# Performance work log

Measured on AMD Instinct MI355X. Metric: run time of the kernel, lower is better.

## Reference

```python
import jax, jax.numpy as jnp
import numpy as np

N_NODES = 50000


def gcn_conv(x, edge_index, W, b):
    """PyG GCNConv: add self-loops, symmetric deg^{-1/2} norm, W then aggregate."""
    n = x.shape[0]
    loops = jnp.arange(n, dtype=edge_index.dtype)
    src = jnp.concatenate([edge_index[0], loops])  # message sources
    dst = jnp.concatenate([edge_index[1], loops])  # aggregation targets
    h = x @ W  # [N, out_dim] -- transform before gather (PyG order)
    deg = jax.ops.segment_sum(jnp.ones_like(dst, dtype=h.dtype), dst, num_segments=n)
    dinv = jnp.where(deg > 0, jax.lax.rsqrt(jnp.maximum(deg, 1.0)), 0.0)
    norm = dinv[src] * dinv[dst]  # [E+N]
    msg = h[src] * norm[:, None]  # gather + normalize
    out = jax.ops.segment_sum(msg, dst, num_segments=n)  # scatter-add
    return out + b


def setup_inputs() -> dict:
    key = jax.random.key(0)
    k1, k2, k3, k4, k5 = jax.random.split(key, 5)
    N, E, D_IN, D_H, D_OUT = N_NODES, 800000, 128, 256, 16
    x = jax.random.normal(k1, (N, D_IN), dtype=jnp.float32)
    edge_index = jax.random.randint(k2, (2, E), 0, N, dtype=jnp.int64)
    s1 = 1.0 / np.sqrt(D_IN)
    s2 = 1.0 / np.sqrt(D_H)
    W1 = jax.random.uniform(k3, (D_IN, D_H), jnp.float32, -s1, s1)
    b1 = jnp.zeros((D_H,), jnp.float32)
    W2 = jax.random.uniform(k4, (D_H, D_OUT), jnp.float32, -s2, s2)
    b2 = jnp.zeros((D_OUT,), jnp.float32)
    return {"x": x, "edge_index": edge_index, "W1": W1, "b1": b1, "W2": W2, "b2": b2}


def reference(x, edge_index, W1, b1, W2, b2):
    h = jax.nn.relu(gcn_conv(x, edge_index, W1, b1))
    # dropout is identity in eval mode
    logits = gcn_conv(h, edge_index, W2, b2)
    return jax.nn.log_softmax(logits, axis=-1)
```

## Files before the change

### kernel.cpp

```cpp
#include <hip/hip_runtime.h>
#include <math.h>

typedef unsigned int uint;
typedef short short8 __attribute__((ext_vector_type(8)));
typedef float floatx4 __attribute__((ext_vector_type(4)));

union U4S8 { uint4 u; short8 s; };

#define CAP 64


__device__ __forceinline__ float blo(uint u) { return __uint_as_float(u << 16); }
__device__ __forceinline__ float bhi(uint u) { return __uint_as_float(u & 0xffff0000u); }
__device__ __forceinline__ uint pack_bf16(float a, float b) {
    uint ua = __float_as_uint(a), ub = __float_as_uint(b);
    ua = (ua + 0x7fffu + ((ua >> 16) & 1u)) >> 16;
    ub = (ub + 0x7fffu + ((ub >> 16) & 1u)) >> 16;
    return ua | (ub << 16);
}
__device__ __forceinline__ unsigned short rb16(float f) {
    uint u = __float_as_uint(f);
    return (unsigned short)((u + 0x7fffu + ((u >> 16) & 1u)) >> 16);
}


__global__ void k_init(int* __restrict__ cnt, int n,
                       const float* __restrict__ W1, const float* __restrict__ W2,
                       uint* __restrict__ W1t, uint* __restrict__ W2t) {
    int i = blockIdx.x * 256 + threadIdx.x;
    if (i < n) cnt[i] = 0;
    if (i < 16384) {
        int nn = i >> 6, kd = i & 63;
        W1t[i] = pack_bf16(W1[(size_t)(2 * kd) * 256 + nn], W1[(size_t)(2 * kd + 1) * 256 + nn]);
    } else if (i < 16384 + 2048) {
        int j = i - 16384;
        int o = j >> 7, kd = j & 127;
        W2t[j] = pack_bf16(W2[(size_t)(2 * kd) * 16 + o], W2[(size_t)(2 * kd + 1) * 16 + o]);
    }
}


__global__ void k_bucket(const int* __restrict__ ei, int E,
                         int* __restrict__ cnt, int* __restrict__ colb) {
    int e = blockIdx.x * 256 + threadIdx.x;
    if (e >= E) return;
    int s = ei[e], t = ei[E + e];
    int slot = atomicAdd(cnt + t, 1);
    if (slot < CAP) colb[(t << 6) + slot] = s;
}


__global__ void k_dinv_cast(const int* __restrict__ cnt, const float2* __restrict__ x2,
                            float* __restrict__ dinv, uint* __restrict__ xsb, int total) {
    int j = blockIdx.x * 256 + threadIdx.x;
    if (j >= total) return;
    int row = j >> 6, lane = j & 63;
    float di = rsqrtf((float)cnt[row] + 1.0f);
    if (lane == 0) dinv[row] = di;
    float2 v = x2[j];
    xsb[j] = pack_bf16(v.x * di, v.y * di);
}


__global__ __launch_bounds__(256) void k_agg_csr128(
    const int* __restrict__ cnt, const int* __restrict__ colb,
    const float* __restrict__ dinv, const uint* __restrict__ xsb,
    uint* __restrict__ outb, int n)
{
    int node = (blockIdx.x * 256 + threadIdx.x) >> 6;
    int lane = threadIdx.x & 63;
    if (node >= n) return;
    float di = dinv[node];
    int deg = min(cnt[node], CAP);
    const int* bucket = colb + (node << 6);
    uint u = xsb[(size_t)node * 64 + lane];
    float ax = blo(u), ay = bhi(u);
    int j = 0;
    for (; j + 8 <= deg; j += 8) {
        int s0 = bucket[j],     s1 = bucket[j + 1], s2 = bucket[j + 2], s3 = bucket[j + 3];
        int s4 = bucket[j + 4], s5 = bucket[j + 5], s6 = bucket[j + 6], s7 = bucket[j + 7];
        uint u0 = xsb[(size_t)s0 * 64 + lane];
        uint u1 = xsb[(size_t)s1 * 64 + lane];
        uint u2 = xsb[(size_t)s2 * 64 + lane];
        uint u3 = xsb[(size_t)s3 * 64 + lane];
        uint u4 = xsb[(size_t)s4 * 64 + lane];
        uint u5 = xsb[(size_t)s5 * 64 + lane];
        uint u6 = xsb[(size_t)s6 * 64 + lane];
        uint u7 = xsb[(size_t)s7 * 64 + lane];
        ax += blo(u0) + blo(u1) + blo(u2) + blo(u3) + blo(u4) + blo(u5) + blo(u6) + blo(u7);
        ay += bhi(u0) + bhi(u1) + bhi(u2) + bhi(u3) + bhi(u4) + bhi(u5) + bhi(u6) + bhi(u7);
    }
    for (; j < deg; ++j) {
        uint uu = xsb[(size_t)bucket[j] * 64 + lane];
        ax += blo(uu); ay += bhi(uu);
    }
    outb[(size_t)node * 64 + lane] = pack_bf16(ax * di, ay * di);
}


__global__ __launch_bounds__(256) void k_gemm_mfma(
    const uint* __restrict__ Ab,
    const uint* __restrict__ W1t,
    const float* __restrict__ b1,
    const uint* __restrict__ W2t,
    const float* __restrict__ dinv,
    float* __restrict__ H2, int M)
{
    __shared__ uint Alds[64 * 68];
    __shared__ uint Hlds[64 * 132];

    const int t    = threadIdx.x;
    const int mb   = blockIdx.x * 64;
    const int wv   = t >> 6;
    const int lane = t & 63;
    const int c    = lane & 15;
    const int q    = lane >> 4;

    #pragma unroll
    for (int it = 0; it < 4; ++it) {
        int i = it * 256 + t;
        int r = i >> 4, cc = i & 15;
        int gr = mb + r;
        uint4 v = make_uint4(0u, 0u, 0u, 0u);
        if (gr < M) v = ((const uint4*)Ab)[(size_t)gr * 16 + cc];
        *(uint4*)&Alds[r * 68 + cc * 4] = v;
    }
    __syncthreads();

    floatx4 acc[4][4];
    #pragma unroll
    for (int i = 0; i < 4; ++i)
        #pragma unroll
        for (int jj = 0; jj < 4; ++jj) acc[i][jj] = (floatx4)0.f;

    #pragma unroll
    for (int kk = 0; kk < 4; ++kk) {
        U4S8 af[4];
        #pragma unroll
        for (int mt = 0; mt < 4; ++mt)
            af[mt].u = *(const uint4*)&Alds[(mt * 16 + c) * 68 + kk * 16 + q * 4];
        #pragma unroll
        for (int nt = 0; nt < 4; ++nt) {
            int n = wv * 64 + nt * 16 + c;
            U4S8 bf;
            bf.u = ((const uint4*)W1t)[(size_t)n * 16 + kk * 4 + q];
            #pragma unroll
            for (int mt = 0; mt < 4; ++mt)
                acc[mt][nt] = __builtin_amdgcn_mfma_f32_16x16x32_bf16(
                    af[mt].s, bf.s, acc[mt][nt], 0, 0, 0);
        }
    }

    float b1v[4];
    #pragma unroll
    for (int nt = 0; nt < 4; ++nt) b1v[nt] = b1[wv * 64 + nt * 16 + c];

    unsigned short* hs = (unsigned short*)Hlds;
    #pragma unroll
    for (int mt = 0; mt < 4; ++mt)
        #pragma unroll
        for (int nt = 0; nt < 4; ++nt)
            #pragma unroll
            for (int r = 0; r < 4; ++r) {
                float hv = fmaxf(acc[mt][nt][r] + b1v[nt], 0.f);
                int row = mt * 16 + q * 4 + r;
                int colc = wv * 64 + nt * 16 + c;
                hs[row * 264 + colc] = rb16(hv);
            }
    __syncthreads();

    floatx4 acc2 = (floatx4)0.f;
    #pragma unroll
    for (int kk = 0; kk < 8; ++kk) {
        U4S8 av, bv;
        av.u = *(const uint4*)&Hlds[(wv * 16 + c) * 132 + kk * 16 + q * 4];
        bv.u = ((const uint4*)W2t)[(size_t)c * 32 + kk * 4 + q];
        acc2 = __builtin_amdgcn_mfma_f32_16x16x32_bf16(av.s, bv.s, acc2, 0, 0, 0);
    }
    #pragma unroll
    for (int r = 0; r < 4; ++r) {
        int gr = mb + wv * 16 + q * 4 + r;
        if (gr < M) H2[(size_t)gr * 16 + c] = acc2[r] * dinv[gr];
    }
}


__global__ __launch_bounds__(256) void k_agg_csr16_lsm(
    const int* __restrict__ cnt, const int* __restrict__ colb,
    const float* __restrict__ dinv, const float* __restrict__ h2s,
    const float* __restrict__ b2, float* __restrict__ out, int n)
{
    int node = (blockIdx.x * 256 + threadIdx.x) >> 4;
    int lane = threadIdx.x & 15;
    if (node >= n) return;
    float di = dinv[node];
    int deg = min(cnt[node], CAP);
    const int* bucket = colb + (node << 6);
    float acc = h2s[(size_t)node * 16 + lane];
    int j = 0;
    for (; j + 8 <= deg; j += 8) {
        int s0 = bucket[j],     s1 = bucket[j + 1], s2 = bucket[j + 2], s3 = bucket[j + 3];
        int s4 = bucket[j + 4], s5 = bucket[j + 5], s6 = bucket[j + 6], s7 = bucket[j + 7];
        float v0 = h2s[(size_t)s0 * 16 + lane];
        float v1 = h2s[(size_t)s1 * 16 + lane];
        float v2 = h2s[(size_t)s2 * 16 + lane];
        float v3 = h2s[(size_t)s3 * 16 + lane];
        float v4 = h2s[(size_t)s4 * 16 + lane];
        float v5 = h2s[(size_t)s5 * 16 + lane];
        float v6 = h2s[(size_t)s6 * 16 + lane];
        float v7 = h2s[(size_t)s7 * 16 + lane];
        acc += v0 + v1 + v2 + v3 + v4 + v5 + v6 + v7;
    }
    for (; j < deg; ++j) acc += h2s[(size_t)bucket[j] * 16 + lane];
    acc = acc * di + b2[lane];
    float m = acc;
    #pragma unroll
    for (int msk = 1; msk < 16; msk <<= 1) m = fmaxf(m, __shfl_xor(m, msk, 16));
    float ex = __expf(acc - m);
    float ssum = ex;
    #pragma unroll
    for (int msk = 1; msk < 16; msk <<= 1) ssum += __shfl_xor(ssum, msk, 16);
    out[(size_t)node * 16 + lane] = acc - m - __logf(ssum);
}


extern "C" void kernel_launch(void* const* d_in, const int* in_sizes, int n_in,
                              void* d_out, int out_size, void* d_ws, size_t ws_size,
                              hipStream_t stream) {
    const float* x  = (const float*)d_in[0];
    const int*   ei = (const int*)d_in[1];
    const float* W1 = (const float*)d_in[2];
    const float* b1 = (const float*)d_in[3];
    const float* W2 = (const float*)d_in[4];
    const float* b2 = (const float*)d_in[5];
    float* out = (float*)d_out;

    const int N = in_sizes[0] / 128;
    const int E = in_sizes[1] / 2;

    float* ws    = (float*)d_ws;
    float* dinv  = ws;
    int*   cnt   = (int*)(ws + 51200);
    int*   colb  = (int*)(ws + 102400);
    uint*  xsb   = (uint*)(ws + 3302400);
    uint*  aggb  = (uint*)(ws + 6502400);
    float* h2s   = ws + 9702400;
    uint*  W1t   = (uint*)(ws + 10502400);
    uint*  W2t   = (uint*)(ws + 10518784);

    const int NB = (N + 255) / 256;

    k_init     <<<NB, 256, 0, stream>>>(cnt, N, W1, W2, W1t, W2t);
    k_bucket   <<<(E + 255) / 256, 256, 0, stream>>>(ei, E, cnt, colb);
    k_dinv_cast<<<(N * 64 + 255) / 256, 256, 0, stream>>>(cnt, (const float2*)x, dinv, xsb, N * 64);

    k_agg_csr128<<<(N * 64 + 255) / 256, 256, 0, stream>>>(cnt, colb, dinv, xsb, aggb, N);
    k_gemm_mfma <<<(N + 63) / 64, 256, 0, stream>>>(aggb, W1t, b1, W2t, dinv, h2s, N);
    k_agg_csr16_lsm<<<(N * 16 + 255) / 256, 256, 0, stream>>>(cnt, colb, dinv, h2s, b2, out, N);
}
```

Baseline: 206.8 us.

## Partition edge buckets per XCD and store 16-bit source indices

The bucketing kernel now picks one of eight partitions from the hardware XCD id, and does its atomic counting and slot writes there. The aim is to cut cross-die contention on the shared degree counters. Column indices drop to 16 bits with a per-partition cap of 24, and both aggregation kernels now walk eight small sub-buckets per node instead of one. This adds eight scattered count reads and gives shorter inner loops with less memory-level parallelism. It also only works while the node count fits in 16 bits, and h2s now reuses the xsb buffer.

```diff
diff --git a/kernel.cpp b/kernel.cpp
--- a/kernel.cpp
+++ b/kernel.cpp
@@ -2,12 +2,14 @@
 #include <math.h>
 
 typedef unsigned int uint;
+typedef unsigned short u16;
 typedef short short8 __attribute__((ext_vector_type(8)));
 typedef float floatx4 __attribute__((ext_vector_type(4)));
 
 union U4S8 { uint4 u; short8 s; };
 
-#define CAP 64
+#define NP   8
+#define CAPP 24
 
 
 __device__ __forceinline__ float blo(uint u) { return __uint_as_float(u << 16); }
@@ -23,12 +25,16 @@
     return (unsigned short)((u + 0x7fffu + ((u >> 16) & 1u)) >> 16);
 }
 
-
-__global__ void k_init(int* __restrict__ cnt, int n,
+__device__ __forceinline__ int xcd_id() {
+    return (int)(__builtin_amdgcn_s_getreg((3 << 11) | 20) & 7);
+}
+
+
+__global__ void k_init(int* __restrict__ cnt8, int n8,
                        const float* __restrict__ W1, const float* __restrict__ W2,
                        uint* __restrict__ W1t, uint* __restrict__ W2t) {
     int i = blockIdx.x * 256 + threadIdx.x;
-    if (i < n) cnt[i] = 0;
+    if (i < n8) cnt8[i] = 0;
     if (i < 16384) {
         int nn = i >> 6, kd = i & 63;
         W1t[i] = pack_bf16(W1[(size_t)(2 * kd) * 256 + nn], W1[(size_t)(2 * kd + 1) * 256 + nn]);
@@ -40,22 +46,28 @@
 }
 
 
-__global__ void k_bucket(const int* __restrict__ ei, int E,
-                         int* __restrict__ cnt, int* __restrict__ colb) {
+__global__ void k_bucket(const int* __restrict__ ei, int E, int N,
+                         int* __restrict__ cnt8, u16* __restrict__ colb) {
     int e = blockIdx.x * 256 + threadIdx.x;
     if (e >= E) return;
+    int part = xcd_id();
     int s = ei[e], t = ei[E + e];
-    int slot = atomicAdd(cnt + t, 1);
-    if (slot < CAP) colb[(t << 6) + slot] = s;
-}
-
-
-__global__ void k_dinv_cast(const int* __restrict__ cnt, const float2* __restrict__ x2,
+    int base = part * N + t;
+    int slot = atomicAdd(cnt8 + base, 1);
+    if (slot < CAPP) colb[(size_t)base * CAPP + slot] = (u16)s;
+}
+
+
+__global__ void k_dinv_cast(const int* __restrict__ cnt8, int n,
+                            const float2* __restrict__ x2,
                             float* __restrict__ dinv, uint* __restrict__ xsb, int total) {
     int j = blockIdx.x * 256 + threadIdx.x;
     if (j >= total) return;
     int row = j >> 6, lane = j & 63;
-    float di = rsqrtf((float)cnt[row] + 1.0f);
+    int deg = 0;
+    #pragma unroll
+    for (int x = 0; x < NP; ++x) deg += cnt8[x * n + row];
+    float di = rsqrtf((float)deg + 1.0f);
     if (lane == 0) dinv[row] = di;
     float2 v = x2[j];
     xsb[j] = pack_bf16(v.x * di, v.y * di);
@@ -63,7 +75,7 @@
 
 
 __global__ __launch_bounds__(256) void k_agg_csr128(
-    const int* __restrict__ cnt, const int* __restrict__ colb,
+    const int* __restrict__ cnt8, const u16* __restrict__ colb,
     const float* __restrict__ dinv, const uint* __restrict__ xsb,
     uint* __restrict__ outb, int n)
 {
@@ -71,28 +83,25 @@
     int lane = threadIdx.x & 63;
     if (node >= n) return;
     float di = dinv[node];
-    int deg = min(cnt[node], CAP);
-    const int* bucket = colb + (node << 6);
     uint u = xsb[(size_t)node * 64 + lane];
     float ax = blo(u), ay = bhi(u);
-    int j = 0;
-    for (; j + 8 <= deg; j += 8) {
-        int s0 = bucket[j],     s1 = bucket[j + 1], s2 = bucket[j + 2], s3 = bucket[j + 3];
-        int s4 = bucket[j + 4], s5 = bucket[j + 5], s6 = bucket[j + 6], s7 = bucket[j + 7];
-        uint u0 = xsb[(size_t)s0 * 64 + lane];
-        uint u1 = xsb[(size_t)s1 * 64 + lane];
-        uint u2 = xsb[(size_t)s2 * 64 + lane];
-        uint u3 = xsb[(size_t)s3 * 64 + lane];
-        uint u4 = xsb[(size_t)s4 * 64 + lane];
-        uint u5 = xsb[(size_t)s5 * 64 + lane];
-        uint u6 = xsb[(size_t)s6 * 64 + lane];
-        uint u7 = xsb[(size_t)s7 * 64 + lane];
-        ax += blo(u0) + blo(u1) + blo(u2) + blo(u3) + blo(u4) + blo(u5) + blo(u6) + blo(u7);
-        ay += bhi(u0) + bhi(u1) + bhi(u2) + bhi(u3) + bhi(u4) + bhi(u5) + bhi(u6) + bhi(u7);
-    }
-    for (; j < deg; ++j) {
-        uint uu = xsb[(size_t)bucket[j] * 64 + lane];
-        ax += blo(uu); ay += bhi(uu);
+    #pragma unroll
+    for (int x = 0; x < NP; ++x) {
+        int base = x * n + node;
+        int deg = min(cnt8[base], CAPP);
+        const u16* bucket = colb + (size_t)base * CAPP;
+        int j = 0;
+        for (; j + 2 <= deg; j += 2) {
+            int s0 = bucket[j], s1 = bucket[j + 1];
+            uint u0 = xsb[(size_t)s0 * 64 + lane];
+            uint u1 = xsb[(size_t)s1 * 64 + lane];
+            ax += blo(u0) + blo(u1);
+            ay += bhi(u0) + bhi(u1);
+        }
+        if (j < deg) {
+            uint uu = xsb[(size_t)bucket[j] * 64 + lane];
+            ax += blo(uu); ay += bhi(uu);
+        }
     }
     outb[(size_t)node * 64 + lane] = pack_bf16(ax * di, ay * di);
 }
@@ -186,7 +195,7 @@
 
 
 __global__ __launch_bounds__(256) void k_agg_csr16_lsm(
-    const int* __restrict__ cnt, const int* __restrict__ colb,
+    const int* __restrict__ cnt8, const u16* __restrict__ colb,
     const float* __restrict__ dinv, const float* __restrict__ h2s,
     const float* __restrict__ b2, float* __restrict__ out, int n)
 {
@@ -194,24 +203,19 @@
     int lane = threadIdx.x & 15;
     if (node >= n) return;
     float di = dinv[node];
-    int deg = min(cnt[node], CAP);
-    const int* bucket = colb + (node << 6);
     float acc = h2s[(size_t)node * 16 + lane];
-    int j = 0;
-    for (; j + 8 <= deg; j += 8) {
-        int s0 = bucket[j],     s1 = bucket[j + 1], s2 = bucket[j + 2], s3 = bucket[j + 3];
-        int s4 = bucket[j + 4], s5 = bucket[j + 5], s6 = bucket[j + 6], s7 = bucket[j + 7];
-        float v0 = h2s[(size_t)s0 * 16 + lane];
-        float v1 = h2s[(size_t)s1 * 16 + lane];
-        float v2 = h2s[(size_t)s2 * 16 + lane];
-        float v3 = h2s[(size_t)s3 * 16 + lane];
-        float v4 = h2s[(size_t)s4 * 16 + lane];
-        float v5 = h2s[(size_t)s5 * 16 + lane];
-        float v6 = h2s[(size_t)s6 * 16 + lane];
-        float v7 = h2s[(size_t)s7 * 16 + lane];
-        acc += v0 + v1 + v2 + v3 + v4 + v5 + v6 + v7;
-    }
-    for (; j < deg; ++j) acc += h2s[(size_t)bucket[j] * 16 + lane];
+    #pragma unroll
+    for (int x = 0; x < NP; ++x) {
+        int base = x * n + node;
+        int deg = min(cnt8[base], CAPP);
+        const u16* bucket = colb + (size_t)base * CAPP;
+        int j = 0;
+        for (; j + 2 <= deg; j += 2) {
+            int s0 = bucket[j], s1 = bucket[j + 1];
+            acc += h2s[(size_t)s0 * 16 + lane] + h2s[(size_t)s1 * 16 + lane];
+        }
+        if (j < deg) acc += h2s[(size_t)bucket[j] * 16 + lane];
+    }
     acc = acc * di + b2[lane];
     float m = acc;
     #pragma unroll
@@ -238,23 +242,21 @@
     const int N = in_sizes[0] / 128;
     const int E = in_sizes[1] / 2;
 
-    float* ws    = (float*)d_ws;
-    float* dinv  = ws;
-    int*   cnt   = (int*)(ws + 51200);
-    int*   colb  = (int*)(ws + 102400);
-    uint*  xsb   = (uint*)(ws + 3302400);
-    uint*  aggb  = (uint*)(ws + 6502400);
-    float* h2s   = ws + 9702400;
-    uint*  W1t   = (uint*)(ws + 10502400);
-    uint*  W2t   = (uint*)(ws + 10518784);
-
-    const int NB = (N + 255) / 256;
-
-    k_init     <<<NB, 256, 0, stream>>>(cnt, N, W1, W2, W1t, W2t);
-    k_bucket   <<<(E + 255) / 256, 256, 0, stream>>>(ei, E, cnt, colb);
-    k_dinv_cast<<<(N * 64 + 255) / 256, 256, 0, stream>>>(cnt, (const float2*)x, dinv, xsb, N * 64);
-
-    k_agg_csr128<<<(N * 64 + 255) / 256, 256, 0, stream>>>(cnt, colb, dinv, xsb, aggb, N);
+    float* ws   = (float*)d_ws;
+    float* dinv = ws;
+    int*   cnt8 = (int*)(ws + 51200);
+    u16*   colb = (u16*)(ws + 460800);
+    uint*  xsb  = (uint*)(ws + 5260800);
+    float* h2s  = (float*)(ws + 5260800);
+    uint*  aggb = (uint*)(ws + 8460800);
+    uint*  W1t  = (uint*)(ws + 11660800);
+    uint*  W2t  = (uint*)(ws + 11677184);
+
+    k_init     <<<(8 * N + 255) / 256, 256, 0, stream>>>(cnt8, 8 * N, W1, W2, W1t, W2t);
+    k_bucket   <<<(E + 255) / 256, 256, 0, stream>>>(ei, E, N, cnt8, colb);
+    k_dinv_cast<<<(N * 64 + 255) / 256, 256, 0, stream>>>(cnt8, N, (const float2*)x, dinv, xsb, N * 64);
+
+    k_agg_csr128<<<(N * 64 + 255) / 256, 256, 0, stream>>>(cnt8, colb, dinv, xsb, aggb, N);
     k_gemm_mfma <<<(N + 63) / 64, 256, 0, stream>>>(aggb, W1t, b1, W2t, dinv, h2s, N);
-    k_agg_csr16_lsm<<<(N * 16 + 255) / 256, 256, 0, stream>>>(cnt, colb, dinv, h2s, b2, out, N);
-}
+    k_agg_csr16_lsm<<<(N * 16 + 255) / 256, 256, 0, stream>>>(cnt8, colb, dinv, h2s, b2, out, N);
+}
```

Result: slower. 254.7 us (+23.2%).
